# Kernel tuning notes

Hardware: AMD Instinct MI355X
Metric: run time of the kernel (lower is better)

Reference implementation:

```python
import jax, jax.numpy as jnp
import numpy as np

D_MODEL = 1024
N_HEADS = 16
D_K = D_MODEL // N_HEADS
SCALE = float(np.sqrt(D_K))


def setup_inputs() -> dict:
    key = jax.random.key(0)
    ks = jax.random.split(key, 12)
    B, S = 2, 2048
    std = 1.0 / np.sqrt(D_MODEL)
    inp = {
        "query": jax.random.normal(ks[0], (B, S, D_MODEL), jnp.float32),
        "key": jax.random.normal(ks[1], (B, S, D_MODEL), jnp.float32),
        "value": jax.random.normal(ks[2], (B, S, D_MODEL), jnp.float32),
        "mask": jnp.ones((B, S), jnp.int32),
        "Wq": jax.random.normal(ks[3], (D_MODEL, D_MODEL), jnp.float32) * std,
        "bq": jnp.zeros((D_MODEL,), jnp.float32),
        "Wk": jax.random.normal(ks[4], (D_MODEL, D_MODEL), jnp.float32) * std,
        "bk": jnp.zeros((D_MODEL,), jnp.float32),
        "Wv": jax.random.normal(ks[5], (D_MODEL, D_MODEL), jnp.float32) * std,
        "bv": jnp.zeros((D_MODEL,), jnp.float32),
        "Wo": jax.random.normal(ks[6], (D_MODEL, D_MODEL), jnp.float32) * std,
        "bo": jnp.zeros((D_MODEL,), jnp.float32),
    }
    return inp


def reference(query, key, value, mask, Wq, bq, Wk, bk, Wv, bv, Wo, bo):
    B, S, _ = query.shape
    # projections -> [B, H, S, d_k]
    def proj(x, W, b):
        return (x @ W.T + b).reshape(B, S, N_HEADS, D_K).transpose(0, 2, 1, 3)

    Q = proj(query, Wq, bq)
    K = proj(key, Wk, bk)
    V = proj(value, Wv, bv)
    # [B, H, Sq, Sk] scores
    scores = jnp.einsum("bhqd,bhkd->bhqk", Q, K) / SCALE
    m = mask[:, None, None, :]  # broadcast over heads and query positions
    scores = jnp.where(m == 0, jnp.float32(-1e9), scores)
    attn = jax.nn.softmax(scores, axis=-1)
    # dropout is identity in eval mode
    context = jnp.einsum("bhqk,bhkd->bhqd", attn, V)
    context = context.transpose(0, 2, 1, 3).reshape(B, S, D_MODEL)
    return context @ Wo.T + bo
```

## Files before the change

kernel.cpp:

```cpp
#include <hip/hip_runtime.h>
#include <stdint.h>

#define D_MODEL 1024
#define NH 16
#define DK 64
#define BATCH 2
#define SEQ 2048
#define MROWS (BATCH*SEQ)

typedef float f32x4 __attribute__((ext_vector_type(4)));
typedef __bf16 bf16x8 __attribute__((ext_vector_type(8)));

#define AS1 __attribute__((address_space(1)))
#define AS3 __attribute__((address_space(3)))

#if __has_builtin(__builtin_amdgcn_exp2f)
#define EXP2F(x) __builtin_amdgcn_exp2f(x)
#else
#define EXP2F(x) exp2f(x)
#endif
#if __has_builtin(__builtin_amdgcn_rcpf)
#define RCPF(x) __builtin_amdgcn_rcpf(x)
#else
#define RCPF(x) (1.0f/(x))
#endif

static __device__ __forceinline__ void gld_lds16(const void* g, void* l) {
    __builtin_amdgcn_global_load_lds((const AS1 unsigned int*)g,
                                     (AS3 unsigned int*)l, 16, 0, 0);
}

static __device__ __forceinline__ unsigned short bfbits(float f) {
    return __builtin_bit_cast(unsigned short, (__bf16)f);
}
static __device__ __forceinline__ unsigned int pk2bf(float a, float b) {
    return (unsigned int)bfbits(a) | ((unsigned int)bfbits(b) << 16);
}

struct PrepArgs {
    const float* src[7];
    unsigned short* dst[7];
    int n4[7];
};

__global__ __launch_bounds__(256) void prep_cvt(PrepArgs a) {
    const int z = blockIdx.y;
    const float4* s = (const float4*)a.src[z];
    uint2* d = (uint2*)a.dst[z];
    const int n = a.n4[z];
    for (int i = blockIdx.x * blockDim.x + threadIdx.x; i < n;
         i += gridDim.x * blockDim.x) {
        float4 v = s[i];
        uint2 o;
        o.x = pk2bf(v.x, v.y);
        o.y = pk2bf(v.z, v.w);
        d[i] = o;
    }
}

struct GemmArgs {
    const unsigned short* A[3];
    const unsigned short* W[3];
    const float* bias[3];
    void* C[3];
    float scale[3];
    int hm[3];
};

template<bool OUT_F32, int BN>
__global__ __launch_bounds__(256) void gemm_bt(GemmArgs g) {
    constexpr int JN = BN / 32;
    __shared__ unsigned short As[128 * 64];
    __shared__ unsigned short Bs[BN * 64];
    const int z = blockIdx.z;
    const char* A = (const char*)g.A[z];
    const char* W = (const char*)g.W[z];
    const float* bias = g.bias[z];
    const float scale = g.scale[z];
    const int hm = g.hm[z];
    const int t = threadIdx.x;
    const int w = t >> 6, lane = t & 63;
    const int m0 = blockIdx.x * 128, n0 = blockIdx.y * BN;
    const int wm = (w >> 1) * 64, wn = (w & 1) * (BN / 2);

    const int srow = t >> 3;
    const int csw = ((t & 7) * 16) ^ ((srow & 7) << 4);
    const char* pA = A + (size_t)(m0 + srow) * 2048 + csw;
    const char* pW = W + (size_t)(n0 + srow) * 2048 + csw;

    f32x4 acc[4][JN];
#pragma unroll
    for (int i = 0; i < 4; ++i)
#pragma unroll
        for (int j = 0; j < JN; ++j)
            acc[i][j] = (f32x4){0.f, 0.f, 0.f, 0.f};

    const int kg16 = (lane >> 4) * 16;
    const int swl = (lane & 7) << 4;

    for (int kt = 0; kt < 16; ++kt) {
        __syncthreads();
#pragma unroll
        for (int p = 0; p < 4; ++p)
            gld_lds16(pA + (size_t)p * (32 * 2048), &As[w * 512 + p * 2048]);
#pragma unroll
        for (int p = 0; p < JN; ++p)
            gld_lds16(pW + (size_t)p * (32 * 2048), &Bs[w * 512 + p * 2048]);
        pA += 128; pW += 128;
        __syncthreads();
#pragma unroll
        for (int ks = 0; ks < 2; ++ks) {
            bf16x8 af[4], bfv[JN];
#pragma unroll
            for (int i = 0; i < 4; ++i) {
                int ra = wm + i * 16 + (lane & 15);
                af[i] = *(const bf16x8*)((const char*)As + ra * 128 +
                                         ((ks * 64 + kg16) ^ swl));
            }
#pragma unroll
            for (int j = 0; j < JN; ++j) {
                int rb = wn + j * 16 + (lane & 15);
                bfv[j] = *(const bf16x8*)((const char*)Bs + rb * 128 +
                                          ((ks * 64 + kg16) ^ swl));
            }
            __builtin_amdgcn_s_setprio(1);
#pragma unroll
            for (int i = 0; i < 4; ++i)
#pragma unroll
                for (int j = 0; j < JN; ++j)
                    acc[i][j] = __builtin_amdgcn_mfma_f32_16x16x32_bf16(
                        af[i], bfv[j], acc[i][j], 0, 0, 0);
            __builtin_amdgcn_s_setprio(0);
        }
    }

    float bj[JN];
#pragma unroll
    for (int j = 0; j < JN; ++j) bj[j] = bias[n0 + wn + j * 16 + (lane & 15)];

    if (hm == 2) {
#pragma unroll
        for (int i = 0; i < 4; ++i) {
            int row0 = m0 + wm + i * 16 + ((lane >> 4) << 2);
            int bb = row0 >> 11, ss0 = row0 & 2047;
#pragma unroll
            for (int j = 0; j < JN; ++j) {
                int col = n0 + wn + j * 16 + (lane & 15);
                int hh = col >> 6, dd = col & 63;
                ushort4 o;
                o.x = bfbits(acc[i][j][0] + bj[j]);
                o.y = bfbits(acc[i][j][1] + bj[j]);
                o.z = bfbits(acc[i][j][2] + bj[j]);
                o.w = bfbits(acc[i][j][3] + bj[j]);
                *(ushort4*)((unsigned short*)g.C[z] +
                            (((size_t)(bb * 16 + hh) * 64 + dd) * 2048 + ss0)) = o;
            }
        }
        return;
    }

#pragma unroll
    for (int i = 0; i < 4; ++i)
#pragma unroll
        for (int r = 0; r < 4; ++r) {
            int row = m0 + wm + i * 16 + (lane >> 4) * 4 + r;
#pragma unroll
            for (int j = 0; j < JN; ++j) {
                int col = n0 + wn + j * 16 + (lane & 15);
                float v = (acc[i][j][r] + bj[j]) * scale;
                if (OUT_F32) {
                    ((float*)g.C[z])[(size_t)row * 1024 + col] = v;
                } else if (hm) {
                    int bb = row >> 11, ss = row & 2047;
                    int hh = col >> 6, dd = col & 63;
                    ((unsigned short*)g.C[z])
                        [(((size_t)(bb * 16 + hh) * 2048) + ss) * 64 + dd] =
                        bfbits(v);
                } else {
                    ((unsigned short*)g.C[z])[(size_t)row * 1024 + col] =
                        bfbits(v);
                }
            }
        }
}

__global__ __launch_bounds__(256) void attn_fwd(
    const unsigned short* __restrict__ Qh,
    const unsigned short* __restrict__ Kh,
    const unsigned short* __restrict__ VtT,
    const int* __restrict__ mask,
    unsigned short* __restrict__ Ctx) {
    __shared__ unsigned short KlA[4096], KlB[4096];
    __shared__ unsigned short VlA[4096], VlB[4096];
    __shared__ unsigned short Plds[4][2048];
    __shared__ int cfl[4];

    const int wg = blockIdx.x + (int)gridDim.x * blockIdx.y;
    const int swzid = (wg & 7) * 64 + (wg >> 3);
    const int qt = swzid & 15, bh = swzid >> 4;
    const int b = bh >> 4, h = bh & 15;

    const int t = threadIdx.x, w = t >> 6, lane = t & 63;
    const int wq0 = w * 32;
    const int g = lane >> 4;
    const int kg16 = g * 16;
    const int swl = (lane & 7) << 4;

    const int* mbase = mask + b * SEQ;
    int myclean = 1;
#pragma unroll
    for (int i = 0; i < 2; ++i) {
        int4 m4 = ((const int4*)mbase)[t + i * 256];
        myclean &= (m4.x != 0) & (m4.y != 0) & (m4.z != 0) & (m4.w != 0);
    }
    int wc = __all(myclean);
    if (lane == 0) cfl[w] = wc;

    const char* Qbase = (const char*)Qh + (size_t)bh * 2048 * 128;
    bf16x8 qf[2][2];
#pragma unroll
    for (int nf = 0; nf < 2; ++nf)
#pragma unroll
        for (int ks = 0; ks < 2; ++ks) {
            int row = qt * 128 + wq0 + nf * 16 + (lane & 15);
            qf[nf][ks] = *(const bf16x8*)(Qbase + (size_t)row * 128 +
                                          ks * 64 + kg16);
        }

    bf16x8 onesf;
#pragma unroll
    for (int j = 0; j < 8; ++j) onesf[j] = (__bf16)1.0f;

    f32x4 cacc[2][4], lacc[2];
#pragma unroll
    for (int i = 0; i < 2; ++i) {
        lacc[i] = (f32x4){0.f, 0.f, 0.f, 0.f};
#pragma unroll
        for (int j = 0; j < 4; ++j) cacc[i][j] = (f32x4){0.f, 0.f, 0.f, 0.f};
    }
    float mstate[2] = {-3e38f, -3e38f};

    const char* Kbyte = (const char*)Kh + (size_t)bh * 2048 * 128;
    const char* Vbyte = (const char*)VtT + (size_t)bh * 64 * 4096;

    const int srow = t >> 3;
    const int csw = ((t & 7) * 16) ^ ((srow & 7) << 4);
    const size_t srow128 = (size_t)srow * 128;
    const size_t srow4096 = (size_t)srow * 4096;

    auto stage = [&](unsigned short* Kd, unsigned short* Vd, int kv0) {
        const char* ks = Kbyte + (size_t)kv0 * 128;
        gld_lds16(ks + srow128 + csw,               Kd + w * 512);
        gld_lds16(ks + srow128 + 32 * 128 + csw,    Kd + 2048 + w * 512);
        const char* vs = Vbyte + (size_t)kv0 * 2;
        gld_lds16(vs + srow4096 + csw,              Vd + w * 512);
        gld_lds16(vs + srow4096 + 32 * 4096 + csw,  Vd + 2048 + w * 512);
    };

    __syncthreads();
    const int clean = cfl[0] & cfl[1] & cfl[2] & cfl[3];

    unsigned short* Pw = &Plds[w][0];

    auto compute = [&](const unsigned short* Kl, const unsigned short* Vl,
                       int kv0) {
        f32x4 sacc[4][2];
#pragma unroll
        for (int i = 0; i < 4; ++i)
#pragma unroll
            for (int j = 0; j < 2; ++j) sacc[i][j] = (f32x4){0.f, 0.f, 0.f, 0.f};
#pragma unroll
        for (int ks = 0; ks < 2; ++ks) {
            bf16x8 kf[4];
#pragma unroll
            for (int mf = 0; mf < 4; ++mf) {
                int r = mf * 16 + (lane & 15);
                kf[mf] = *(const bf16x8*)((const char*)Kl + r * 128 +
                                          ((ks * 64 + kg16) ^ swl));
            }
            __builtin_amdgcn_s_setprio(1);
#pragma unroll
            for (int mf = 0; mf < 4; ++mf)
#pragma unroll
                for (int nf = 0; nf < 2; ++nf)
                    sacc[mf][nf] = __builtin_amdgcn_mfma_f32_16x16x32_bf16(
                        kf[mf], qf[nf][ks], sacc[mf][nf], 0, 0, 0);
            __builtin_amdgcn_s_setprio(0);
        }

        if (!clean) {
#pragma unroll
            for (int mf = 0; mf < 4; ++mf) {
                int4 mk = *(const int4*)(mbase + kv0 + mf * 16 + g * 4);
#pragma unroll
                for (int r = 0; r < 4; ++r) {
                    if ((&mk.x)[r] == 0) {
                        sacc[mf][0][r] = -1e9f;
                        sacc[mf][1][r] = -1e9f;
                    }
                }
            }
        }

        float vm[2];
#pragma unroll
        for (int nf = 0; nf < 2; ++nf) {
            float a0 = fmaxf(fmaxf(sacc[0][nf][0], sacc[0][nf][1]),
                             fmaxf(sacc[0][nf][2], sacc[0][nf][3]));
            float a1 = fmaxf(fmaxf(sacc[1][nf][0], sacc[1][nf][1]),
                             fmaxf(sacc[1][nf][2], sacc[1][nf][3]));
            float a2 = fmaxf(fmaxf(sacc[2][nf][0], sacc[2][nf][1]),
                             fmaxf(sacc[2][nf][2], sacc[2][nf][3]));
            float a3 = fmaxf(fmaxf(sacc[3][nf][0], sacc[3][nf][1]),
                             fmaxf(sacc[3][nf][2], sacc[3][nf][3]));
            float m4 = fmaxf(fmaxf(a0, a1), fmaxf(a2, a3));
            m4 = fmaxf(m4, __shfl_xor(m4, 16));
            vm[nf] = fmaxf(m4, __shfl_xor(m4, 32));
        }
        if (!__all((vm[0] <= mstate[0] + 8.f) & (vm[1] <= mstate[1] + 8.f))) {
            float sc[2];
#pragma unroll
            for (int nf = 0; nf < 2; ++nf) {
                float mnew = fmaxf(mstate[nf], vm[nf]);
                sc[nf] = EXP2F(mstate[nf] - mnew);
                mstate[nf] = mnew;
            }
#pragma unroll
            for (int mq = 0; mq < 2; ++mq)
#pragma unroll
                for (int r = 0; r < 4; ++r) {
                    float scb = __shfl(sc[mq], g * 4 + r);
                    lacc[mq][r] *= scb;
#pragma unroll
                    for (int nd = 0; nd < 4; ++nd) cacc[mq][nd][r] *= scb;
                }
        }

#pragma unroll
        for (int nf = 0; nf < 2; ++nf) {
            float mn = mstate[nf];
#pragma unroll
            for (int mf = 0; mf < 4; ++mf) {
                unsigned int d0 = pk2bf(EXP2F(sacc[mf][nf][0] - mn),
                                        EXP2F(sacc[mf][nf][1] - mn));
                unsigned int d1 = pk2bf(EXP2F(sacc[mf][nf][2] - mn),
                                        EXP2F(sacc[mf][nf][3] - mn));
                int q = nf * 16 + (lane & 15);
                int kb = mf * 32 + g * 8;
                unsigned long long pv =
                    (unsigned long long)d0 | ((unsigned long long)d1 << 32);
                *(unsigned long long*)((char*)Pw + q * 128 +
                                       (kb ^ ((q & 7) << 4))) = pv;
            }
        }

#pragma unroll
        for (int ks = 0; ks < 2; ++ks) {
            bf16x8 pa[2], vf[4];
#pragma unroll
            for (int mq = 0; mq < 2; ++mq) {
                int r = mq * 16 + (lane & 15);
                pa[mq] = *(const bf16x8*)((const char*)Pw + r * 128 +
                                          ((ks * 64 + kg16) ^ swl));
            }
#pragma unroll
            for (int nd = 0; nd < 4; ++nd) {
                int r = nd * 16 + (lane & 15);
                vf[nd] = *(const bf16x8*)((const char*)Vl + r * 128 +
                                          ((ks * 64 + kg16) ^ swl));
            }
            __builtin_amdgcn_s_setprio(1);
#pragma unroll
            for (int mq = 0; mq < 2; ++mq) {
                lacc[mq] = __builtin_amdgcn_mfma_f32_16x16x32_bf16(
                    pa[mq], onesf, lacc[mq], 0, 0, 0);
#pragma unroll
                for (int nd = 0; nd < 4; ++nd)
                    cacc[mq][nd] = __builtin_amdgcn_mfma_f32_16x16x32_bf16(
                        pa[mq], vf[nd], cacc[mq][nd], 0, 0, 0);
            }
            __builtin_amdgcn_s_setprio(0);
        }
    };

    stage(KlA, VlA, 0);
    __syncthreads();
    for (int i = 0; i < 16; ++i) {
        const int kv0 = i * 128;
        if (kv0 + 64 < SEQ) stage(KlB, VlB, kv0 + 64);
        compute(KlA, VlA, kv0);
        __syncthreads();
        if (kv0 + 128 < SEQ) stage(KlA, VlA, kv0 + 128);
        compute(KlB, VlB, kv0 + 64);
        __syncthreads();
    }

#pragma unroll
    for (int mq = 0; mq < 2; ++mq)
#pragma unroll
        for (int r = 0; r < 4; ++r) {
            float inv = RCPF(lacc[mq][r]);
            size_t row = (size_t)b * SEQ + qt * 128 + wq0 + mq * 16 +
                         g * 4 + r;
#pragma unroll
            for (int nd = 0; nd < 4; ++nd) {
                int col = h * 64 + nd * 16 + (lane & 15);
                Ctx[row * 1024 + col] = bfbits(cacc[mq][nd][r] * inv);
            }
        }
}

extern "C" void kernel_launch(void* const* d_in, const int* in_sizes, int n_in,
                              void* d_out, int out_size, void* d_ws, size_t ws_size,
                              hipStream_t stream) {
    const float* q   = (const float*)d_in[0];
    const float* k   = (const float*)d_in[1];
    const float* v   = (const float*)d_in[2];
    const int* mask  = (const int*)d_in[3];
    const float* Wq  = (const float*)d_in[4];
    const float* bq  = (const float*)d_in[5];
    const float* Wk  = (const float*)d_in[6];
    const float* bk  = (const float*)d_in[7];
    const float* Wv  = (const float*)d_in[8];
    const float* bv  = (const float*)d_in[9];
    const float* Wo  = (const float*)d_in[10];
    const float* bo  = (const float*)d_in[11];

    unsigned short* ws = (unsigned short*)d_ws;
    const size_t NX = (size_t)MROWS * D_MODEL;
    const size_t NW = (size_t)D_MODEL * D_MODEL;
    unsigned short* Xq  = ws;
    unsigned short* Xk  = Xq + NX;
    unsigned short* Xv  = Xk + NX;
    unsigned short* Wqb = Xv + NX;
    unsigned short* Wkb = Wqb + NW;
    unsigned short* Wvb = Wkb + NW;
    unsigned short* Wob = Wvb + NW;
    unsigned short* Qhd = Wob + NW;
    unsigned short* Khd = Qhd + NX;
    unsigned short* Vtt = Khd + NX;
    unsigned short* Cx  = Vtt + NX;

    PrepArgs pa;
    pa.src[0] = q;  pa.src[1] = k;  pa.src[2] = v;
    pa.src[3] = Wq; pa.src[4] = Wk; pa.src[5] = Wv; pa.src[6] = Wo;
    pa.dst[0] = Xq;  pa.dst[1] = Xk;  pa.dst[2] = Xv;
    pa.dst[3] = Wqb; pa.dst[4] = Wkb; pa.dst[5] = Wvb; pa.dst[6] = Wob;
    for (int i = 0; i < 3; ++i) pa.n4[i] = (int)(NX / 4);
    for (int i = 3; i < 7; ++i) pa.n4[i] = (int)(NW / 4);
    prep_cvt<<<dim3(256, 7), dim3(256), 0, stream>>>(pa);

    GemmArgs gq;
    gq.A[0] = Xq;  gq.A[1] = Xk;  gq.A[2] = Xv;
    gq.W[0] = Wqb; gq.W[1] = Wkb; gq.W[2] = Wvb;
    gq.bias[0] = bq; gq.bias[1] = bk; gq.bias[2] = bv;
    gq.C[0] = Qhd; gq.C[1] = Khd; gq.C[2] = Vtt;
    gq.scale[0] = 0.125f * 1.44269504088896340736f;
    gq.scale[1] = 1.f; gq.scale[2] = 1.f;
    gq.hm[0] = 1; gq.hm[1] = 1; gq.hm[2] = 2;
    gemm_bt<false, 128><<<dim3(32, 8, 3), dim3(256), 0, stream>>>(gq);

    attn_fwd<<<dim3(16, 32), dim3(256), 0, stream>>>(Qhd, Khd, Vtt, mask, Cx);

    GemmArgs go;
    go.A[0] = Cx; go.W[0] = Wob; go.bias[0] = bo; go.C[0] = d_out;
    go.scale[0] = 1.f; go.hm[0] = 0;
    go.A[1] = go.A[2] = nullptr; go.W[1] = go.W[2] = nullptr;
    go.bias[1] = go.bias[2] = nullptr; go.C[1] = go.C[2] = nullptr;
    go.scale[1] = go.scale[2] = 1.f; go.hm[1] = go.hm[2] = 0;
    gemm_bt<true, 64><<<dim3(32, 16, 1), dim3(256), 0, stream>>>(go);
}
```

Baseline: 227.8 us.

## Split attention KV range across two blocks and merge partials in combine kernel

The attention kernel now splits each query tile's key/value sequence into two halves, processed by separate workgroups (grid z=2). Each writes an unnormalized bf16 partial output plus its running max and sum, and a new combine kernel rescales and merges them. This doubles the attention grid from 512 to 1024 blocks to fill more CUs on MI355X, at the cost of extra partial-output traffic, an additional launch, and bf16 rounding of the unnormalized partials. The output projection GEMM also switches to 64x128 tiles with a different grid shape.

```diff
diff --git a/kernel.cpp b/kernel.cpp
--- a/kernel.cpp
+++ b/kernel.cpp
@@ -35,6 +35,9 @@
 }
 static __device__ __forceinline__ unsigned int pk2bf(float a, float b) {
     return (unsigned int)bfbits(a) | ((unsigned int)bfbits(b) << 16);
+}
+static __device__ __forceinline__ float bf2f(unsigned int u) {
+    return __builtin_bit_cast(float, u << 16);
 }
 
 struct PrepArgs {
@@ -67,10 +70,11 @@
     int hm[3];
 };
 
-template<bool OUT_F32, int BN>
+template<bool OUT_F32, int BM, int BN>
 __global__ __launch_bounds__(256) void gemm_bt(GemmArgs g) {
+    constexpr int IM = BM / 32;
     constexpr int JN = BN / 32;
-    __shared__ unsigned short As[128 * 64];
+    __shared__ unsigned short As[BM * 64];
     __shared__ unsigned short Bs[BN * 64];
     const int z = blockIdx.z;
     const char* A = (const char*)g.A[z];
@@ -80,28 +84,29 @@
     const int hm = g.hm[z];
     const int t = threadIdx.x;
     const int w = t >> 6, lane = t & 63;
-    const int m0 = blockIdx.x * 128, n0 = blockIdx.y * BN;
-    const int wm = (w >> 1) * 64, wn = (w & 1) * (BN / 2);
+    const int m0 = blockIdx.x * BM, n0 = blockIdx.y * BN;
+    const int wm = (w >> 1) * (BM / 2), wn = (w & 1) * (BN / 2);
 
     const int srow = t >> 3;
     const int csw = ((t & 7) * 16) ^ ((srow & 7) << 4);
     const char* pA = A + (size_t)(m0 + srow) * 2048 + csw;
     const char* pW = W + (size_t)(n0 + srow) * 2048 + csw;
 
-    f32x4 acc[4][JN];
-#pragma unroll
-    for (int i = 0; i < 4; ++i)
+    f32x4 acc[IM][JN];
+#pragma unroll
+    for (int i = 0; i < IM; ++i)
 #pragma unroll
         for (int j = 0; j < JN; ++j)
             acc[i][j] = (f32x4){0.f, 0.f, 0.f, 0.f};
 
-    const int kg16 = (lane >> 4) * 16;
+    const int g4 = lane >> 4;
+    const int kg16 = g4 * 16;
     const int swl = (lane & 7) << 4;
 
     for (int kt = 0; kt < 16; ++kt) {
         __syncthreads();
 #pragma unroll
-        for (int p = 0; p < 4; ++p)
+        for (int p = 0; p < IM; ++p)
             gld_lds16(pA + (size_t)p * (32 * 2048), &As[w * 512 + p * 2048]);
 #pragma unroll
         for (int p = 0; p < JN; ++p)
@@ -110,9 +115,9 @@
         __syncthreads();
 #pragma unroll
         for (int ks = 0; ks < 2; ++ks) {
-            bf16x8 af[4], bfv[JN];
-#pragma unroll
-            for (int i = 0; i < 4; ++i) {
+            bf16x8 af[IM], bfv[JN];
+#pragma unroll
+            for (int i = 0; i < IM; ++i) {
                 int ra = wm + i * 16 + (lane & 15);
                 af[i] = *(const bf16x8*)((const char*)As + ra * 128 +
                                          ((ks * 64 + kg16) ^ swl));
@@ -125,7 +130,7 @@
             }
             __builtin_amdgcn_s_setprio(1);
 #pragma unroll
-            for (int i = 0; i < 4; ++i)
+            for (int i = 0; i < IM; ++i)
 #pragma unroll
                 for (int j = 0; j < JN; ++j)
                     acc[i][j] = __builtin_amdgcn_mfma_f32_16x16x32_bf16(
@@ -140,8 +145,8 @@
 
     if (hm == 2) {
 #pragma unroll
-        for (int i = 0; i < 4; ++i) {
-            int row0 = m0 + wm + i * 16 + ((lane >> 4) << 2);
+        for (int i = 0; i < IM; ++i) {
+            int row0 = m0 + wm + i * 16 + (g4 << 2);
             int bb = row0 >> 11, ss0 = row0 & 2047;
 #pragma unroll
             for (int j = 0; j < JN; ++j) {
@@ -160,10 +165,10 @@
     }
 
 #pragma unroll
-    for (int i = 0; i < 4; ++i)
+    for (int i = 0; i < IM; ++i)
 #pragma unroll
         for (int r = 0; r < 4; ++r) {
-            int row = m0 + wm + i * 16 + (lane >> 4) * 4 + r;
+            int row = m0 + wm + i * 16 + g4 * 4 + r;
 #pragma unroll
             for (int j = 0; j < JN; ++j) {
                 int col = n0 + wn + j * 16 + (lane & 15);
@@ -189,16 +194,20 @@
     const unsigned short* __restrict__ Kh,
     const unsigned short* __restrict__ VtT,
     const int* __restrict__ mask,
-    unsigned short* __restrict__ Ctx) {
+    unsigned short* __restrict__ Opart,
+    float* __restrict__ Mlf,
+    float* __restrict__ Llf) {
     __shared__ unsigned short KlA[4096], KlB[4096];
     __shared__ unsigned short VlA[4096], VlB[4096];
     __shared__ unsigned short Plds[4][2048];
     __shared__ int cfl[4];
 
-    const int wg = blockIdx.x + (int)gridDim.x * blockIdx.y;
-    const int swzid = (wg & 7) * 64 + (wg >> 3);
-    const int qt = swzid & 15, bh = swzid >> 4;
+    const int wg = blockIdx.x + (int)gridDim.x *
+                   (blockIdx.y + (int)gridDim.y * blockIdx.z);
+    const int swz = (wg & 7) * 128 + (wg >> 3);
+    const int sp = swz & 1, qt = (swz >> 1) & 15, bh = swz >> 5;
     const int b = bh >> 4, h = bh & 15;
+    const int kvb = sp * 1024;
 
     const int t = threadIdx.x, w = t >> 6, lane = t & 63;
     const int wq0 = w * 32;
@@ -207,12 +216,8 @@
     const int swl = (lane & 7) << 4;
 
     const int* mbase = mask + b * SEQ;
-    int myclean = 1;
-#pragma unroll
-    for (int i = 0; i < 2; ++i) {
-        int4 m4 = ((const int4*)mbase)[t + i * 256];
-        myclean &= (m4.x != 0) & (m4.y != 0) & (m4.z != 0) & (m4.w != 0);
-    }
+    int4 m4 = ((const int4*)(mbase + kvb))[t];
+    int myclean = (m4.x != 0) & (m4.y != 0) & (m4.z != 0) & (m4.w != 0);
     int wc = __all(myclean);
     if (lane == 0) cfl[w] = wc;
 
@@ -313,9 +318,9 @@
                              fmaxf(sacc[2][nf][2], sacc[2][nf][3]));
             float a3 = fmaxf(fmaxf(sacc[3][nf][0], sacc[3][nf][1]),
                              fmaxf(sacc[3][nf][2], sacc[3][nf][3]));
-            float m4 = fmaxf(fmaxf(a0, a1), fmaxf(a2, a3));
-            m4 = fmaxf(m4, __shfl_xor(m4, 16));
-            vm[nf] = fmaxf(m4, __shfl_xor(m4, 32));
+            float m4x = fmaxf(fmaxf(a0, a1), fmaxf(a2, a3));
+            m4x = fmaxf(m4x, __shfl_xor(m4x, 16));
+            vm[nf] = fmaxf(m4x, __shfl_xor(m4x, 32));
         }
         if (!__all((vm[0] <= mstate[0] + 8.f) & (vm[1] <= mstate[1] + 8.f))) {
             float sc[2];
@@ -383,14 +388,14 @@
         }
     };
 
-    stage(KlA, VlA, 0);
+    stage(KlA, VlA, kvb);
     __syncthreads();
-    for (int i = 0; i < 16; ++i) {
-        const int kv0 = i * 128;
-        if (kv0 + 64 < SEQ) stage(KlB, VlB, kv0 + 64);
+    for (int i = 0; i < 8; ++i) {
+        const int kv0 = kvb + i * 128;
+        stage(KlB, VlB, kv0 + 64);
         compute(KlA, VlA, kv0);
         __syncthreads();
-        if (kv0 + 128 < SEQ) stage(KlA, VlA, kv0 + 128);
+        if (i < 7) stage(KlA, VlA, kv0 + 128);
         compute(KlB, VlB, kv0 + 64);
         __syncthreads();
     }
@@ -399,15 +404,60 @@
     for (int mq = 0; mq < 2; ++mq)
 #pragma unroll
         for (int r = 0; r < 4; ++r) {
-            float inv = RCPF(lacc[mq][r]);
-            size_t row = (size_t)b * SEQ + qt * 128 + wq0 + mq * 16 +
-                         g * 4 + r;
+            int sq = qt * 128 + wq0 + mq * 16 + g * 4 + r;
+            size_t row = (size_t)(sp * 4096 + b * 2048 + sq);
 #pragma unroll
             for (int nd = 0; nd < 4; ++nd) {
                 int col = h * 64 + nd * 16 + (lane & 15);
-                Ctx[row * 1024 + col] = bfbits(cacc[mq][nd][r] * inv);
-            }
-        }
+                Opart[row * 1024 + col] = bfbits(cacc[mq][nd][r]);
+            }
+        }
+    if ((lane & 15) == 0) {
+#pragma unroll
+        for (int mq = 0; mq < 2; ++mq)
+#pragma unroll
+            for (int r = 0; r < 4; ++r)
+                Llf[sp * 65536 + bh * 2048 + qt * 128 + wq0 + mq * 16 +
+                    g * 4 + r] = lacc[mq][r];
+    }
+    if (g == 0) {
+#pragma unroll
+        for (int mq = 0; mq < 2; ++mq)
+            Mlf[sp * 65536 + bh * 2048 + qt * 128 + wq0 + mq * 16 +
+                (lane & 15)] = mstate[mq];
+    }
+}
+
+__global__ __launch_bounds__(256) void attn_combine(
+    const unsigned short* __restrict__ Op,
+    const float* __restrict__ Mlf,
+    const float* __restrict__ Llf,
+    unsigned short* __restrict__ Cx) {
+    const int idx = blockIdx.x * 256 + threadIdx.x;
+    const int row = idx >> 7;
+    const int c8 = (idx & 127) << 3;
+    const int b = row >> 11, s = row & 2047, h = c8 >> 6;
+    const int li = (b * 16 + h) * 2048 + s;
+    const float m1 = Mlf[li], m2 = Mlf[65536 + li];
+    const float l1 = Llf[li], l2 = Llf[65536 + li];
+    const float mx = fmaxf(m1, m2);
+    float w1 = EXP2F(m1 - mx), w2 = EXP2F(m2 - mx);
+    const float inv = RCPF(fmaf(l1, w1, l2 * w2));
+    w1 *= inv; w2 *= inv;
+    const uint4 o1 = *(const uint4*)(Op + (size_t)row * 1024 + c8);
+    const uint4 o2 = *(const uint4*)(Op + (size_t)(4096 + row) * 1024 + c8);
+    uint4 o;
+    unsigned int rr[4];
+#pragma unroll
+    for (int j = 0; j < 4; ++j) {
+        unsigned int a = ((const unsigned int*)&o1)[j];
+        unsigned int c = ((const unsigned int*)&o2)[j];
+        float x0 = bf2f(a & 0xffffu) * w1 + bf2f(c & 0xffffu) * w2;
+        float x1 = bf2f(a >> 16) * w1 + bf2f(c >> 16) * w2;
+        rr[j] = pk2bf(x0, x1);
+    }
+    o.x = rr[0]; o.y = rr[1]; o.z = rr[2]; o.w = rr[3];
+    *(uint4*)(Cx + (size_t)row * 1024 + c8) = o;
 }
 
 extern "C" void kernel_launch(void* const* d_in, const int* in_sizes, int n_in,
@@ -458,9 +508,15 @@
     gq.scale[0] = 0.125f * 1.44269504088896340736f;
     gq.scale[1] = 1.f; gq.scale[2] = 1.f;
     gq.hm[0] = 1; gq.hm[1] = 1; gq.hm[2] = 2;
-    gemm_bt<false, 128><<<dim3(32, 8, 3), dim3(256), 0, stream>>>(gq);
-
-    attn_fwd<<<dim3(16, 32), dim3(256), 0, stream>>>(Qhd, Khd, Vtt, mask, Cx);
+    gemm_bt<false, 128, 128><<<dim3(32, 8, 3), dim3(256), 0, stream>>>(gq);
+
+    unsigned short* Opart = Xq;
+    float* Mlf = (float*)Xv;
+    float* Llf = Mlf + 2 * 65536;
+    attn_fwd<<<dim3(16, 32, 2), dim3(256), 0, stream>>>(
+        Qhd, Khd, Vtt, mask, Opart, Mlf, Llf);
+
+    attn_combine<<<dim3(2048), dim3(256), 0, stream>>>(Opart, Mlf, Llf, Cx);
 
     GemmArgs go;
     go.A[0] = Cx; go.W[0] = Wob; go.bias[0] = bo; go.C[0] = d_out;
@@ -468,5 +524,5 @@
     go.A[1] = go.A[2] = nullptr; go.W[1] = go.W[2] = nullptr;
     go.bias[1] = go.bias[2] = nullptr; go.C[1] = go.C[2] = nullptr;
     go.scale[1] = go.scale[2] = 1.f; go.hm[1] = go.hm[2] = 0;
-    gemm_bt<true, 64><<<dim3(32, 16, 1), dim3(256), 0, stream>>>(go);
-}
+    gemm_bt<true, 64, 128><<<dim3(64, 8, 1), dim3(256), 0, stream>>>(go);
+}
```

Measured after the change: 244.1 us. 7.2% more time.

## Add double-buffered 256x256 8-wave GEMM kernel for QKV projection

Applied to the files above, without the earlier changes.

Replaces the 128x128 single-buffered QKV projection GEMM with a new 512-thread kernel using 256x256 tiles. It double-buffers the LDS tiles and interleaves the next K-tile's global-to-LDS loads with four MFMA phases, using explicit waitcnt and barriers. The goal is to hide global load latency behind the matrix math and raise data reuse per tile. The cost is fewer workgroups (192) and heavy LDS and register use, which may limit occupancy or leave CUs underfilled. The old gemm_bt is made generic in BM, its head-major transposed store path is removed, and it is kept for the output projection.

```diff
diff --git a/kernel.cpp b/kernel.cpp
--- a/kernel.cpp
+++ b/kernel.cpp
@@ -67,10 +67,11 @@
     int hm[3];
 };
 
-template<bool OUT_F32, int BN>
+template<bool OUT_F32, int BM, int BN>
 __global__ __launch_bounds__(256) void gemm_bt(GemmArgs g) {
+    constexpr int IM = BM / 32;
     constexpr int JN = BN / 32;
-    __shared__ unsigned short As[128 * 64];
+    __shared__ unsigned short As[BM * 64];
     __shared__ unsigned short Bs[BN * 64];
     const int z = blockIdx.z;
     const char* A = (const char*)g.A[z];
@@ -80,28 +81,29 @@
     const int hm = g.hm[z];
     const int t = threadIdx.x;
     const int w = t >> 6, lane = t & 63;
-    const int m0 = blockIdx.x * 128, n0 = blockIdx.y * BN;
-    const int wm = (w >> 1) * 64, wn = (w & 1) * (BN / 2);
+    const int m0 = blockIdx.x * BM, n0 = blockIdx.y * BN;
+    const int wm = (w >> 1) * (BM / 2), wn = (w & 1) * (BN / 2);
 
     const int srow = t >> 3;
     const int csw = ((t & 7) * 16) ^ ((srow & 7) << 4);
     const char* pA = A + (size_t)(m0 + srow) * 2048 + csw;
     const char* pW = W + (size_t)(n0 + srow) * 2048 + csw;
 
-    f32x4 acc[4][JN];
-#pragma unroll
-    for (int i = 0; i < 4; ++i)
+    f32x4 acc[IM][JN];
+#pragma unroll
+    for (int i = 0; i < IM; ++i)
 #pragma unroll
         for (int j = 0; j < JN; ++j)
             acc[i][j] = (f32x4){0.f, 0.f, 0.f, 0.f};
 
-    const int kg16 = (lane >> 4) * 16;
+    const int g4 = lane >> 4;
+    const int kg16 = g4 * 16;
     const int swl = (lane & 7) << 4;
 
     for (int kt = 0; kt < 16; ++kt) {
         __syncthreads();
 #pragma unroll
-        for (int p = 0; p < 4; ++p)
+        for (int p = 0; p < IM; ++p)
             gld_lds16(pA + (size_t)p * (32 * 2048), &As[w * 512 + p * 2048]);
 #pragma unroll
         for (int p = 0; p < JN; ++p)
@@ -110,9 +112,9 @@
         __syncthreads();
 #pragma unroll
         for (int ks = 0; ks < 2; ++ks) {
-            bf16x8 af[4], bfv[JN];
-#pragma unroll
-            for (int i = 0; i < 4; ++i) {
+            bf16x8 af[IM], bfv[JN];
+#pragma unroll
+            for (int i = 0; i < IM; ++i) {
                 int ra = wm + i * 16 + (lane & 15);
                 af[i] = *(const bf16x8*)((const char*)As + ra * 128 +
                                          ((ks * 64 + kg16) ^ swl));
@@ -125,7 +127,7 @@
             }
             __builtin_amdgcn_s_setprio(1);
 #pragma unroll
-            for (int i = 0; i < 4; ++i)
+            for (int i = 0; i < IM; ++i)
 #pragma unroll
                 for (int j = 0; j < JN; ++j)
                     acc[i][j] = __builtin_amdgcn_mfma_f32_16x16x32_bf16(
@@ -138,32 +140,11 @@
 #pragma unroll
     for (int j = 0; j < JN; ++j) bj[j] = bias[n0 + wn + j * 16 + (lane & 15)];
 
-    if (hm == 2) {
-#pragma unroll
-        for (int i = 0; i < 4; ++i) {
-            int row0 = m0 + wm + i * 16 + ((lane >> 4) << 2);
-            int bb = row0 >> 11, ss0 = row0 & 2047;
-#pragma unroll
-            for (int j = 0; j < JN; ++j) {
-                int col = n0 + wn + j * 16 + (lane & 15);
-                int hh = col >> 6, dd = col & 63;
-                ushort4 o;
-                o.x = bfbits(acc[i][j][0] + bj[j]);
-                o.y = bfbits(acc[i][j][1] + bj[j]);
-                o.z = bfbits(acc[i][j][2] + bj[j]);
-                o.w = bfbits(acc[i][j][3] + bj[j]);
-                *(ushort4*)((unsigned short*)g.C[z] +
-                            (((size_t)(bb * 16 + hh) * 64 + dd) * 2048 + ss0)) = o;
-            }
-        }
-        return;
-    }
-
-#pragma unroll
-    for (int i = 0; i < 4; ++i)
+#pragma unroll
+    for (int i = 0; i < IM; ++i)
 #pragma unroll
         for (int r = 0; r < 4; ++r) {
-            int row = m0 + wm + i * 16 + (lane >> 4) * 4 + r;
+            int row = m0 + wm + i * 16 + g4 * 4 + r;
 #pragma unroll
             for (int j = 0; j < JN; ++j) {
                 int col = n0 + wn + j * 16 + (lane & 15);
@@ -184,6 +165,204 @@
         }
 }
 
+__global__ __launch_bounds__(512, 2) void gemm_8p(GemmArgs g) {
+    __shared__ unsigned short Al[2][256 * 64];
+    __shared__ unsigned short Bl[2][256 * 64];
+    const int z = blockIdx.z;
+    const char* A = (const char*)g.A[z];
+    const char* W = (const char*)g.W[z];
+    const float* bias = g.bias[z];
+    const float scale = g.scale[z];
+    const int hm = g.hm[z];
+    const int t = threadIdx.x;
+    const int w = t >> 6, lane = t & 63;
+    const int m0 = blockIdx.x * 256, n0 = blockIdx.y * 256;
+    const int wm = (w >> 2) * 128, wn = (w & 3) * 64;
+    const int g4 = lane >> 4, kg16 = g4 * 16, swl = (lane & 7) << 4;
+
+    const int csw = ((t & 7) * 16) ^ (((t >> 3) & 7) << 4);
+    const char* pA = A + (size_t)(m0 + (t >> 3)) * 2048 + csw;
+    const char* pW = W + (size_t)(n0 + (t >> 3)) * 2048 + csw;
+
+    auto stA = [&](int kt, int buf, int half) {
+        const char* s = pA + (size_t)half * (128 * 2048) + kt * 128;
+        unsigned short* d = &Al[buf][(half * 128 + w * 8) * 64];
+        gld_lds16(s, d);
+        gld_lds16(s + (size_t)64 * 2048, d + 64 * 64);
+    };
+    auto stB = [&](int kt, int buf, int half) {
+        const char* s = pW + (size_t)half * (128 * 2048) + kt * 128;
+        unsigned short* d = &Bl[buf][(half * 128 + w * 8) * 64];
+        gld_lds16(s, d);
+        gld_lds16(s + (size_t)64 * 2048, d + 64 * 64);
+    };
+
+    f32x4 acc[8][4];
+#pragma unroll
+    for (int i = 0; i < 8; ++i)
+#pragma unroll
+        for (int j = 0; j < 4; ++j) acc[i][j] = (f32x4){0.f, 0.f, 0.f, 0.f};
+
+    bf16x8 afq[4][2], bq0[2][2], bq1[2][2];
+
+    stA(0, 0, 0); stA(0, 0, 1); stB(0, 0, 0); stB(0, 0, 1);
+
+    for (int kt = 0; kt < 16; ++kt) {
+        const int bc = kt & 1, bn2 = bc ^ 1;
+        const char* Ab = (const char*)Al[bc];
+        const char* Bb = (const char*)Bl[bc];
+        const bool more = (kt + 1) < 16;
+
+        if (more) {
+            stA(kt + 1, bn2, 0);
+            asm volatile("s_waitcnt vmcnt(2)" ::: "memory");
+        } else {
+            asm volatile("s_waitcnt vmcnt(0)" ::: "memory");
+        }
+        __builtin_amdgcn_sched_barrier(0);
+        __builtin_amdgcn_s_barrier();
+#pragma unroll
+        for (int i = 0; i < 4; ++i)
+#pragma unroll
+            for (int ks = 0; ks < 2; ++ks) {
+                int ra = wm + i * 16 + (lane & 15);
+                afq[i][ks] = *(const bf16x8*)(Ab + ra * 128 +
+                                              ((ks * 64 + kg16) ^ swl));
+            }
+#pragma unroll
+        for (int j = 0; j < 2; ++j)
+#pragma unroll
+            for (int ks = 0; ks < 2; ++ks) {
+                int rb = wn + j * 16 + (lane & 15);
+                bq0[j][ks] = *(const bf16x8*)(Bb + rb * 128 +
+                                              ((ks * 64 + kg16) ^ swl));
+            }
+        __builtin_amdgcn_s_barrier();
+        asm volatile("s_waitcnt lgkmcnt(0)" ::: "memory");
+        __builtin_amdgcn_sched_barrier(0);
+        __builtin_amdgcn_s_setprio(1);
+#pragma unroll
+        for (int ks = 0; ks < 2; ++ks)
+#pragma unroll
+            for (int i = 0; i < 4; ++i)
+#pragma unroll
+                for (int j = 0; j < 2; ++j)
+                    acc[i][j] = __builtin_amdgcn_mfma_f32_16x16x32_bf16(
+                        afq[i][ks], bq0[j][ks], acc[i][j], 0, 0, 0);
+        __builtin_amdgcn_s_setprio(0);
+        __builtin_amdgcn_s_barrier();
+
+        if (more) stA(kt + 1, bn2, 1);
+#pragma unroll
+        for (int j = 0; j < 2; ++j)
+#pragma unroll
+            for (int ks = 0; ks < 2; ++ks) {
+                int rb = wn + 32 + j * 16 + (lane & 15);
+                bq1[j][ks] = *(const bf16x8*)(Bb + rb * 128 +
+                                              ((ks * 64 + kg16) ^ swl));
+            }
+        __builtin_amdgcn_s_barrier();
+        asm volatile("s_waitcnt lgkmcnt(0)" ::: "memory");
+        __builtin_amdgcn_sched_barrier(0);
+        __builtin_amdgcn_s_setprio(1);
+#pragma unroll
+        for (int ks = 0; ks < 2; ++ks)
+#pragma unroll
+            for (int i = 0; i < 4; ++i)
+#pragma unroll
+                for (int j = 0; j < 2; ++j)
+                    acc[i][2 + j] = __builtin_amdgcn_mfma_f32_16x16x32_bf16(
+                        afq[i][ks], bq1[j][ks], acc[i][2 + j], 0, 0, 0);
+        __builtin_amdgcn_s_setprio(0);
+        __builtin_amdgcn_s_barrier();
+
+        if (more) stB(kt + 1, bn2, 0);
+#pragma unroll
+        for (int i = 0; i < 4; ++i)
+#pragma unroll
+            for (int ks = 0; ks < 2; ++ks) {
+                int ra = wm + 64 + i * 16 + (lane & 15);
+                afq[i][ks] = *(const bf16x8*)(Ab + ra * 128 +
+                                              ((ks * 64 + kg16) ^ swl));
+            }
+        __builtin_amdgcn_s_barrier();
+        asm volatile("s_waitcnt lgkmcnt(0)" ::: "memory");
+        __builtin_amdgcn_sched_barrier(0);
+        __builtin_amdgcn_s_setprio(1);
+#pragma unroll
+        for (int ks = 0; ks < 2; ++ks)
+#pragma unroll
+            for (int i = 0; i < 4; ++i)
+#pragma unroll
+                for (int j = 0; j < 2; ++j)
+                    acc[4 + i][2 + j] = __builtin_amdgcn_mfma_f32_16x16x32_bf16(
+                        afq[i][ks], bq1[j][ks], acc[4 + i][2 + j], 0, 0, 0);
+        __builtin_amdgcn_s_setprio(0);
+        __builtin_amdgcn_s_barrier();
+
+        if (more) stB(kt + 1, bn2, 1);
+        __builtin_amdgcn_s_barrier();
+        __builtin_amdgcn_s_setprio(1);
+#pragma unroll
+        for (int ks = 0; ks < 2; ++ks)
+#pragma unroll
+            for (int i = 0; i < 4; ++i)
+#pragma unroll
+                for (int j = 0; j < 2; ++j)
+                    acc[4 + i][j] = __builtin_amdgcn_mfma_f32_16x16x32_bf16(
+                        afq[i][ks], bq0[j][ks], acc[4 + i][j], 0, 0, 0);
+        __builtin_amdgcn_s_setprio(0);
+        __builtin_amdgcn_s_barrier();
+    }
+
+    float bj[4];
+#pragma unroll
+    for (int j = 0; j < 4; ++j) bj[j] = bias[n0 + wn + j * 16 + (lane & 15)];
+
+    if (hm == 2) {
+#pragma unroll
+        for (int i = 0; i < 8; ++i) {
+            int row0 = m0 + wm + i * 16 + (g4 << 2);
+            int bb = row0 >> 11, ss0 = row0 & 2047;
+#pragma unroll
+            for (int j = 0; j < 4; ++j) {
+                int col = n0 + wn + j * 16 + (lane & 15);
+                int hh = col >> 6, dd = col & 63;
+                ushort4 o;
+                o.x = bfbits(acc[i][j][0] + bj[j]);
+                o.y = bfbits(acc[i][j][1] + bj[j]);
+                o.z = bfbits(acc[i][j][2] + bj[j]);
+                o.w = bfbits(acc[i][j][3] + bj[j]);
+                *(ushort4*)((unsigned short*)g.C[z] +
+                            (((size_t)(bb * 16 + hh) * 64 + dd) * 2048 + ss0)) = o;
+            }
+        }
+        return;
+    }
+
+#pragma unroll
+    for (int i = 0; i < 8; ++i)
+#pragma unroll
+        for (int r = 0; r < 4; ++r) {
+            int row = m0 + wm + i * 16 + g4 * 4 + r;
+#pragma unroll
+            for (int j = 0; j < 4; ++j) {
+                int col = n0 + wn + j * 16 + (lane & 15);
+                float v = (acc[i][j][r] + bj[j]) * scale;
+                if (hm) {
+                    int bb = row >> 11, ss = row & 2047;
+                    int hh = col >> 6, dd = col & 63;
+                    ((unsigned short*)g.C[z])
+                        [(((size_t)(bb * 16 + hh) * 2048) + ss) * 64 + dd] =
+                        bfbits(v);
+                } else {
+                    ((unsigned short*)g.C[z])[(size_t)row * 1024 + col] =
+                        bfbits(v);
+                }
+            }
+        }
+}
+
 __global__ __launch_bounds__(256) void attn_fwd(
     const unsigned short* __restrict__ Qh,
     const unsigned short* __restrict__ Kh,
@@ -313,9 +492,9 @@
                              fmaxf(sacc[2][nf][2], sacc[2][nf][3]));
             float a3 = fmaxf(fmaxf(sacc[3][nf][0], sacc[3][nf][1]),
                              fmaxf(sacc[3][nf][2], sacc[3][nf][3]));
-            float m4 = fmaxf(fmaxf(a0, a1), fmaxf(a2, a3));
-            m4 = fmaxf(m4, __shfl_xor(m4, 16));
-            vm[nf] = fmaxf(m4, __shfl_xor(m4, 32));
+            float m4x = fmaxf(fmaxf(a0, a1), fmaxf(a2, a3));
+            m4x = fmaxf(m4x, __shfl_xor(m4x, 16));
+            vm[nf] = fmaxf(m4x, __shfl_xor(m4x, 32));
         }
         if (!__all((vm[0] <= mstate[0] + 8.f) & (vm[1] <= mstate[1] + 8.f))) {
             float sc[2];
@@ -458,7 +637,7 @@
     gq.scale[0] = 0.125f * 1.44269504088896340736f;
     gq.scale[1] = 1.f; gq.scale[2] = 1.f;
     gq.hm[0] = 1; gq.hm[1] = 1; gq.hm[2] = 2;
-    gemm_bt<false, 128><<<dim3(32, 8, 3), dim3(256), 0, stream>>>(gq);
+    gemm_8p<<<dim3(16, 4, 3), dim3(512), 0, stream>>>(gq);
 
     attn_fwd<<<dim3(16, 32), dim3(256), 0, stream>>>(Qhd, Khd, Vtt, mask, Cx);
 
@@ -468,5 +647,5 @@
     go.A[1] = go.A[2] = nullptr; go.W[1] = go.W[2] = nullptr;
     go.bias[1] = go.bias[2] = nullptr; go.C[1] = go.C[2] = nullptr;
     go.scale[1] = go.scale[2] = 1.f; go.hm[1] = go.hm[2] = 0;
-    gemm_bt<true, 64><<<dim3(32, 16, 1), dim3(256), 0, stream>>>(go);
-}
+    gemm_bt<true, 128, 64><<<dim3(32, 16, 1), dim3(256), 0, stream>>>(go);
+}
```

After: 244.2 us. 1.07x slower.

## Rewrite attention with 32x32x16 MFMA and register-resident P via permlane swap

Applied to the files above, without the earlier changes.

The attention kernel moves from 16x16x32 MFMAs with P written to and re-read from LDS to 32x32x16 MFMAs. The probabilities stay in registers and are rearranged into the A-operand layout with v_permlane32_swap. Row sums are now computed with scalar adds and a cross-half shuffle instead of an extra MFMA against a ones vector, and the per-wave P LDS buffer is removed. This targets LDS traffic and MFMA issue overhead, at the cost of more per-row shuffles for rescaling and output and reliance on inline asm for the lane swap. The GEMM template gains a BM parameter, but the launches keep the same tile sizes.

```diff
diff --git a/kernel.cpp b/kernel.cpp
--- a/kernel.cpp
+++ b/kernel.cpp
@@ -9,6 +9,7 @@
 #define MROWS (BATCH*SEQ)
 
 typedef float f32x4 __attribute__((ext_vector_type(4)));
+typedef float f32x16 __attribute__((ext_vector_type(16)));
 typedef __bf16 bf16x8 __attribute__((ext_vector_type(8)));
 
 #define AS1 __attribute__((address_space(1)))
@@ -25,6 +26,10 @@
 #define RCPF(x) (1.0f/(x))
 #endif
 
+#define PERMSWAP(a, b) \
+    asm volatile("s_nop 1\n\tv_permlane32_swap_b32 %0, %1" \
+                 : "+v"(a), "+v"(b))
+
 static __device__ __forceinline__ void gld_lds16(const void* g, void* l) {
     __builtin_amdgcn_global_load_lds((const AS1 unsigned int*)g,
                                      (AS3 unsigned int*)l, 16, 0, 0);
@@ -35,6 +40,14 @@
 }
 static __device__ __forceinline__ unsigned int pk2bf(float a, float b) {
     return (unsigned int)bfbits(a) | ((unsigned int)bfbits(b) << 16);
+}
+
+static __device__ __forceinline__ float vmax16(const f32x16& v) {
+    float a = fmaxf(fmaxf(v[0], v[1]), fmaxf(v[2], v[3]));
+    float b = fmaxf(fmaxf(v[4], v[5]), fmaxf(v[6], v[7]));
+    float c = fmaxf(fmaxf(v[8], v[9]), fmaxf(v[10], v[11]));
+    float d = fmaxf(fmaxf(v[12], v[13]), fmaxf(v[14], v[15]));
+    return fmaxf(fmaxf(a, b), fmaxf(c, d));
 }
 
 struct PrepArgs {
@@ -67,10 +80,11 @@
     int hm[3];
 };
 
-template<bool OUT_F32, int BN>
+template<bool OUT_F32, int BM, int BN>
 __global__ __launch_bounds__(256) void gemm_bt(GemmArgs g) {
+    constexpr int IM = BM / 32;
     constexpr int JN = BN / 32;
-    __shared__ unsigned short As[128 * 64];
+    __shared__ unsigned short As[BM * 64];
     __shared__ unsigned short Bs[BN * 64];
     const int z = blockIdx.z;
     const char* A = (const char*)g.A[z];
@@ -80,28 +94,29 @@
     const int hm = g.hm[z];
     const int t = threadIdx.x;
     const int w = t >> 6, lane = t & 63;
-    const int m0 = blockIdx.x * 128, n0 = blockIdx.y * BN;
-    const int wm = (w >> 1) * 64, wn = (w & 1) * (BN / 2);
+    const int m0 = blockIdx.x * BM, n0 = blockIdx.y * BN;
+    const int wm = (w >> 1) * (BM / 2), wn = (w & 1) * (BN / 2);
 
     const int srow = t >> 3;
     const int csw = ((t & 7) * 16) ^ ((srow & 7) << 4);
     const char* pA = A + (size_t)(m0 + srow) * 2048 + csw;
     const char* pW = W + (size_t)(n0 + srow) * 2048 + csw;
 
-    f32x4 acc[4][JN];
-#pragma unroll
-    for (int i = 0; i < 4; ++i)
+    f32x4 acc[IM][JN];
+#pragma unroll
+    for (int i = 0; i < IM; ++i)
 #pragma unroll
         for (int j = 0; j < JN; ++j)
             acc[i][j] = (f32x4){0.f, 0.f, 0.f, 0.f};
 
-    const int kg16 = (lane >> 4) * 16;
+    const int g4 = lane >> 4;
+    const int kg16 = g4 * 16;
     const int swl = (lane & 7) << 4;
 
     for (int kt = 0; kt < 16; ++kt) {
         __syncthreads();
 #pragma unroll
-        for (int p = 0; p < 4; ++p)
+        for (int p = 0; p < IM; ++p)
             gld_lds16(pA + (size_t)p * (32 * 2048), &As[w * 512 + p * 2048]);
 #pragma unroll
         for (int p = 0; p < JN; ++p)
@@ -110,9 +125,9 @@
         __syncthreads();
 #pragma unroll
         for (int ks = 0; ks < 2; ++ks) {
-            bf16x8 af[4], bfv[JN];
-#pragma unroll
-            for (int i = 0; i < 4; ++i) {
+            bf16x8 af[IM], bfv[JN];
+#pragma unroll
+            for (int i = 0; i < IM; ++i) {
                 int ra = wm + i * 16 + (lane & 15);
                 af[i] = *(const bf16x8*)((const char*)As + ra * 128 +
                                          ((ks * 64 + kg16) ^ swl));
@@ -125,7 +140,7 @@
             }
             __builtin_amdgcn_s_setprio(1);
 #pragma unroll
-            for (int i = 0; i < 4; ++i)
+            for (int i = 0; i < IM; ++i)
 #pragma unroll
                 for (int j = 0; j < JN; ++j)
                     acc[i][j] = __builtin_amdgcn_mfma_f32_16x16x32_bf16(
@@ -140,8 +155,8 @@
 
     if (hm == 2) {
 #pragma unroll
-        for (int i = 0; i < 4; ++i) {
-            int row0 = m0 + wm + i * 16 + ((lane >> 4) << 2);
+        for (int i = 0; i < IM; ++i) {
+            int row0 = m0 + wm + i * 16 + (g4 << 2);
             int bb = row0 >> 11, ss0 = row0 & 2047;
 #pragma unroll
             for (int j = 0; j < JN; ++j) {
@@ -160,10 +175,10 @@
     }
 
 #pragma unroll
-    for (int i = 0; i < 4; ++i)
+    for (int i = 0; i < IM; ++i)
 #pragma unroll
         for (int r = 0; r < 4; ++r) {
-            int row = m0 + wm + i * 16 + (lane >> 4) * 4 + r;
+            int row = m0 + wm + i * 16 + g4 * 4 + r;
 #pragma unroll
             for (int j = 0; j < JN; ++j) {
                 int col = n0 + wn + j * 16 + (lane & 15);
@@ -192,7 +207,6 @@
     unsigned short* __restrict__ Ctx) {
     __shared__ unsigned short KlA[4096], KlB[4096];
     __shared__ unsigned short VlA[4096], VlB[4096];
-    __shared__ unsigned short Plds[4][2048];
     __shared__ int cfl[4];
 
     const int wg = blockIdx.x + (int)gridDim.x * blockIdx.y;
@@ -201,10 +215,8 @@
     const int b = bh >> 4, h = bh & 15;
 
     const int t = threadIdx.x, w = t >> 6, lane = t & 63;
-    const int wq0 = w * 32;
-    const int g = lane >> 4;
-    const int kg16 = g * 16;
-    const int swl = (lane & 7) << 4;
+    const int hi = lane >> 5, q5 = lane & 31;
+    const int swl5 = (q5 & 7) << 4;
 
     const int* mbase = mask + b * SEQ;
     int myclean = 1;
@@ -217,28 +229,17 @@
     if (lane == 0) cfl[w] = wc;
 
     const char* Qbase = (const char*)Qh + (size_t)bh * 2048 * 128;
-    bf16x8 qf[2][2];
-#pragma unroll
-    for (int nf = 0; nf < 2; ++nf)
-#pragma unroll
-        for (int ks = 0; ks < 2; ++ks) {
-            int row = qt * 128 + wq0 + nf * 16 + (lane & 15);
-            qf[nf][ks] = *(const bf16x8*)(Qbase + (size_t)row * 128 +
-                                          ks * 64 + kg16);
-        }
-
-    bf16x8 onesf;
-#pragma unroll
-    for (int j = 0; j < 8; ++j) onesf[j] = (__bf16)1.0f;
-
-    f32x4 cacc[2][4], lacc[2];
-#pragma unroll
-    for (int i = 0; i < 2; ++i) {
-        lacc[i] = (f32x4){0.f, 0.f, 0.f, 0.f};
-#pragma unroll
-        for (int j = 0; j < 4; ++j) cacc[i][j] = (f32x4){0.f, 0.f, 0.f, 0.f};
-    }
-    float mstate[2] = {-3e38f, -3e38f};
+    const int qrow = qt * 128 + w * 32 + q5;
+    bf16x8 qf[4];
+#pragma unroll
+    for (int t4 = 0; t4 < 4; ++t4)
+        qf[t4] = *(const bf16x8*)(Qbase + (size_t)qrow * 128 +
+                                  t4 * 32 + hi * 16);
+
+    f32x16 cacc[2];
+#pragma unroll
+    for (int r = 0; r < 16; ++r) { cacc[0][r] = 0.f; cacc[1][r] = 0.f; }
+    float mstate = -3e38f, lstate = 0.f;
 
     const char* Kbyte = (const char*)Kh + (size_t)bh * 2048 * 128;
     const char* Vbyte = (const char*)VtT + (size_t)bh * 64 * 4096;
@@ -260,125 +261,86 @@
     __syncthreads();
     const int clean = cfl[0] & cfl[1] & cfl[2] & cfl[3];
 
-    unsigned short* Pw = &Plds[w][0];
-
     auto compute = [&](const unsigned short* Kl, const unsigned short* Vl,
                        int kv0) {
-        f32x4 sacc[4][2];
-#pragma unroll
-        for (int i = 0; i < 4; ++i)
-#pragma unroll
-            for (int j = 0; j < 2; ++j) sacc[i][j] = (f32x4){0.f, 0.f, 0.f, 0.f};
-#pragma unroll
-        for (int ks = 0; ks < 2; ++ks) {
-            bf16x8 kf[4];
-#pragma unroll
-            for (int mf = 0; mf < 4; ++mf) {
-                int r = mf * 16 + (lane & 15);
-                kf[mf] = *(const bf16x8*)((const char*)Kl + r * 128 +
-                                          ((ks * 64 + kg16) ^ swl));
-            }
+        f32x16 sacc[2];
+#pragma unroll
+        for (int r = 0; r < 16; ++r) { sacc[0][r] = 0.f; sacc[1][r] = 0.f; }
+#pragma unroll
+        for (int t4 = 0; t4 < 4; ++t4) {
+            int off = (t4 * 32 + hi * 16) ^ swl5;
+            bf16x8 kf0 = *(const bf16x8*)((const char*)Kl + q5 * 128 + off);
+            bf16x8 kf1 = *(const bf16x8*)((const char*)Kl + (32 + q5) * 128 + off);
             __builtin_amdgcn_s_setprio(1);
-#pragma unroll
-            for (int mf = 0; mf < 4; ++mf)
-#pragma unroll
-                for (int nf = 0; nf < 2; ++nf)
-                    sacc[mf][nf] = __builtin_amdgcn_mfma_f32_16x16x32_bf16(
-                        kf[mf], qf[nf][ks], sacc[mf][nf], 0, 0, 0);
+            sacc[0] = __builtin_amdgcn_mfma_f32_32x32x16_bf16(
+                kf0, qf[t4], sacc[0], 0, 0, 0);
+            sacc[1] = __builtin_amdgcn_mfma_f32_32x32x16_bf16(
+                kf1, qf[t4], sacc[1], 0, 0, 0);
             __builtin_amdgcn_s_setprio(0);
         }
 
         if (!clean) {
 #pragma unroll
-            for (int mf = 0; mf < 4; ++mf) {
-                int4 mk = *(const int4*)(mbase + kv0 + mf * 16 + g * 4);
-#pragma unroll
-                for (int r = 0; r < 4; ++r) {
-                    if ((&mk.x)[r] == 0) {
-                        sacc[mf][0][r] = -1e9f;
-                        sacc[mf][1][r] = -1e9f;
-                    }
+            for (int kb = 0; kb < 2; ++kb)
+#pragma unroll
+                for (int r = 0; r < 16; ++r) {
+                    int key = kb * 32 + (r & 3) + 8 * (r >> 2) + 4 * hi;
+                    if (mbase[kv0 + key] == 0) sacc[kb][r] = -1e9f;
                 }
-            }
-        }
-
-        float vm[2];
-#pragma unroll
-        for (int nf = 0; nf < 2; ++nf) {
-            float a0 = fmaxf(fmaxf(sacc[0][nf][0], sacc[0][nf][1]),
-                             fmaxf(sacc[0][nf][2], sacc[0][nf][3]));
-            float a1 = fmaxf(fmaxf(sacc[1][nf][0], sacc[1][nf][1]),
-                             fmaxf(sacc[1][nf][2], sacc[1][nf][3]));
-            float a2 = fmaxf(fmaxf(sacc[2][nf][0], sacc[2][nf][1]),
-                             fmaxf(sacc[2][nf][2], sacc[2][nf][3]));
-            float a3 = fmaxf(fmaxf(sacc[3][nf][0], sacc[3][nf][1]),
-                             fmaxf(sacc[3][nf][2], sacc[3][nf][3]));
-            float m4 = fmaxf(fmaxf(a0, a1), fmaxf(a2, a3));
-            m4 = fmaxf(m4, __shfl_xor(m4, 16));
-            vm[nf] = fmaxf(m4, __shfl_xor(m4, 32));
-        }
-        if (!__all((vm[0] <= mstate[0] + 8.f) & (vm[1] <= mstate[1] + 8.f))) {
-            float sc[2];
-#pragma unroll
-            for (int nf = 0; nf < 2; ++nf) {
-                float mnew = fmaxf(mstate[nf], vm[nf]);
-                sc[nf] = EXP2F(mstate[nf] - mnew);
-                mstate[nf] = mnew;
-            }
-#pragma unroll
-            for (int mq = 0; mq < 2; ++mq)
-#pragma unroll
-                for (int r = 0; r < 4; ++r) {
-                    float scb = __shfl(sc[mq], g * 4 + r);
-                    lacc[mq][r] *= scb;
-#pragma unroll
-                    for (int nd = 0; nd < 4; ++nd) cacc[mq][nd][r] *= scb;
-                }
-        }
-
-#pragma unroll
-        for (int nf = 0; nf < 2; ++nf) {
-            float mn = mstate[nf];
-#pragma unroll
-            for (int mf = 0; mf < 4; ++mf) {
-                unsigned int d0 = pk2bf(EXP2F(sacc[mf][nf][0] - mn),
-                                        EXP2F(sacc[mf][nf][1] - mn));
-                unsigned int d1 = pk2bf(EXP2F(sacc[mf][nf][2] - mn),
-                                        EXP2F(sacc[mf][nf][3] - mn));
-                int q = nf * 16 + (lane & 15);
-                int kb = mf * 32 + g * 8;
-                unsigned long long pv =
-                    (unsigned long long)d0 | ((unsigned long long)d1 << 32);
-                *(unsigned long long*)((char*)Pw + q * 128 +
-                                       (kb ^ ((q & 7) << 4))) = pv;
-            }
-        }
-
-#pragma unroll
-        for (int ks = 0; ks < 2; ++ks) {
-            bf16x8 pa[2], vf[4];
-#pragma unroll
-            for (int mq = 0; mq < 2; ++mq) {
-                int r = mq * 16 + (lane & 15);
-                pa[mq] = *(const bf16x8*)((const char*)Pw + r * 128 +
-                                          ((ks * 64 + kg16) ^ swl));
-            }
-#pragma unroll
-            for (int nd = 0; nd < 4; ++nd) {
-                int r = nd * 16 + (lane & 15);
-                vf[nd] = *(const bf16x8*)((const char*)Vl + r * 128 +
-                                          ((ks * 64 + kg16) ^ swl));
-            }
+        }
+
+        float vm = fmaxf(vmax16(sacc[0]), vmax16(sacc[1]));
+        vm = fmaxf(vm, __shfl_xor(vm, 32));
+
+        if (!__all(vm <= mstate + 8.f)) {
+            float mnew = fmaxf(mstate, vm);
+            float sc = EXP2F(mstate - mnew);
+            mstate = mnew;
+            lstate *= sc;
+#pragma unroll
+            for (int r = 0; r < 16; ++r) {
+                float scb = __shfl(sc, (r & 3) + 8 * (r >> 2) + 4 * hi);
+                cacc[0][r] *= scb;
+                cacc[1][r] *= scb;
+            }
+        }
+
+        const float mn = mstate;
+        float ssum = 0.f;
+        unsigned int Ap[2][4], Bp[2][4];
+#pragma unroll
+        for (int kb = 0; kb < 2; ++kb)
+#pragma unroll
+            for (int si = 0; si < 4; ++si) {
+                float e0 = EXP2F(sacc[kb][4 * si + 0] - mn);
+                float e1 = EXP2F(sacc[kb][4 * si + 1] - mn);
+                float e2 = EXP2F(sacc[kb][4 * si + 2] - mn);
+                float e3 = EXP2F(sacc[kb][4 * si + 3] - mn);
+                ssum += (e0 + e1) + (e2 + e3);
+                Ap[kb][si] = pk2bf(e0, e1);
+                Bp[kb][si] = pk2bf(e2, e3);
+            }
+        ssum += __shfl_xor(ssum, 32);
+        lstate += ssum;
+
+#pragma unroll
+        for (int ct = 0; ct < 4; ++ct) {
+            const int kb = ct >> 1, sA = (ct & 1) * 2;
+            unsigned int w0 = Ap[kb][sA], w2 = Ap[kb][sA + 1];
+            unsigned int w1 = Bp[kb][sA], w3 = Bp[kb][sA + 1];
+            PERMSWAP(w0, w2);
+            PERMSWAP(w1, w3);
+            union { unsigned int u[4]; bf16x8 v; } pa;
+            pa.u[0] = w0; pa.u[1] = w1; pa.u[2] = w2; pa.u[3] = w3;
+
+            int off = (ct * 32 + hi * 16) ^ swl5;
+            bf16x8 vf0 = *(const bf16x8*)((const char*)Vl + q5 * 128 + off);
+            bf16x8 vf1 = *(const bf16x8*)((const char*)Vl + (32 + q5) * 128 + off);
             __builtin_amdgcn_s_setprio(1);
-#pragma unroll
-            for (int mq = 0; mq < 2; ++mq) {
-                lacc[mq] = __builtin_amdgcn_mfma_f32_16x16x32_bf16(
-                    pa[mq], onesf, lacc[mq], 0, 0, 0);
-#pragma unroll
-                for (int nd = 0; nd < 4; ++nd)
-                    cacc[mq][nd] = __builtin_amdgcn_mfma_f32_16x16x32_bf16(
-                        pa[mq], vf[nd], cacc[mq][nd], 0, 0, 0);
-            }
+            cacc[0] = __builtin_amdgcn_mfma_f32_32x32x16_bf16(
+                pa.v, vf0, cacc[0], 0, 0, 0);
+            cacc[1] = __builtin_amdgcn_mfma_f32_32x32x16_bf16(
+                pa.v, vf1, cacc[1], 0, 0, 0);
             __builtin_amdgcn_s_setprio(0);
         }
     };
@@ -395,19 +357,15 @@
         __syncthreads();
     }
 
-#pragma unroll
-    for (int mq = 0; mq < 2; ++mq)
-#pragma unroll
-        for (int r = 0; r < 4; ++r) {
-            float inv = RCPF(lacc[mq][r]);
-            size_t row = (size_t)b * SEQ + qt * 128 + wq0 + mq * 16 +
-                         g * 4 + r;
-#pragma unroll
-            for (int nd = 0; nd < 4; ++nd) {
-                int col = h * 64 + nd * 16 + (lane & 15);
-                Ctx[row * 1024 + col] = bfbits(cacc[mq][nd][r] * inv);
-            }
-        }
+    const float inv = RCPF(lstate);
+#pragma unroll
+    for (int r = 0; r < 16; ++r) {
+        int cr = (r & 3) + 8 * (r >> 2) + 4 * hi;
+        float invr = __shfl(inv, cr);
+        size_t row = (size_t)b * SEQ + qt * 128 + w * 32 + cr;
+        Ctx[row * 1024 + h * 64 + q5]      = bfbits(cacc[0][r] * invr);
+        Ctx[row * 1024 + h * 64 + 32 + q5] = bfbits(cacc[1][r] * invr);
+    }
 }
 
 extern "C" void kernel_launch(void* const* d_in, const int* in_sizes, int n_in,
@@ -458,7 +416,7 @@
     gq.scale[0] = 0.125f * 1.44269504088896340736f;
     gq.scale[1] = 1.f; gq.scale[2] = 1.f;
     gq.hm[0] = 1; gq.hm[1] = 1; gq.hm[2] = 2;
-    gemm_bt<false, 128><<<dim3(32, 8, 3), dim3(256), 0, stream>>>(gq);
+    gemm_bt<false, 128, 128><<<dim3(32, 8, 3), dim3(256), 0, stream>>>(gq);
 
     attn_fwd<<<dim3(16, 32), dim3(256), 0, stream>>>(Qhd, Khd, Vtt, mask, Cx);
 
@@ -468,5 +426,5 @@
     go.A[1] = go.A[2] = nullptr; go.W[1] = go.W[2] = nullptr;
     go.bias[1] = go.bias[2] = nullptr; go.C[1] = go.C[2] = nullptr;
     go.scale[1] = go.scale[2] = 1.f; go.hm[1] = go.hm[2] = 0;
-    gemm_bt<true, 64><<<dim3(32, 16, 1), dim3(256), 0, stream>>>(go);
-}
+    gemm_bt<true, 128, 64><<<dim3(32, 16, 1), dim3(256), 0, stream>>>(go);
+}
```

Result: slower. 234.5 us (+3.0%).
